# Kernel optimization log

Measured on AMD Instinct MI355X. Metric: run time of the kernel, lower is better.

Reference implementation:

```python
import jax, jax.numpy as jnp
import numpy as np

TWO_PI = 2.0 * np.pi


def setup_inputs() -> dict:
    key = jax.random.key(0)
    ks = jax.random.split(key, 6)
    n1 = n2 = n3 = 20
    nk, ni, nspin = 4, 16, 2
    # Invertible, physically plausible lattice (~8 Bohr cubic cell + jitter)
    A = jnp.eye(3, dtype=jnp.float32) * 8.0 + 0.05 * jax.random.normal(ks[0], (3, 3), jnp.float32)
    k_grid = 0.1 * jax.random.normal(ks[1], (nk, 3), jnp.float32)
    cg_real = jax.random.normal(ks[2], (nspin, nk, ni, n1, n2, n3), jnp.float32)
    cg_imag = jax.random.normal(ks[3], (nspin, nk, ni, n1, n2, n3), jnp.float32)
    # Real-space evaluation grid: fractional coords in [0,1)^3 mapped through A
    frac = jax.random.uniform(ks[4], (n1, n2, n3, 3), jnp.float32)
    r = frac @ A
    return {"A": A, "k_grid": k_grid, "cg_real": cg_real, "cg_imag": cg_imag, "r": r}


def reference(A, k_grid, cg_real, cg_imag, r):
    # cg: [spin, nk, ni, n1, n2, n3] complex plane-wave coefficients
    cg = cg_real + 1j * cg_imag
    n1, n2, n3 = cg.shape[-3:]
    # Integer FFT frequency mesh m -> reciprocal-lattice vectors G = m @ B,
    # B rows are reciprocal basis: B = 2*pi * inv(A)^T  (A rows = lattice vecs)
    f1 = jnp.fft.fftfreq(n1) * n1
    f2 = jnp.fft.fftfreq(n2) * n2
    f3 = jnp.fft.fftfreq(n3) * n3
    m = jnp.stack(jnp.meshgrid(f1, f2, f3, indexing="ij"), axis=-1).astype(A.dtype)  # [n1,n2,n3,3]
    B = TWO_PI * jnp.linalg.inv(A).T
    G = (m @ B).reshape(-1, 3)                      # [nG, 3]
    vol = jnp.abs(jnp.linalg.det(A))
    Rf = r.reshape(-1, 3)                           # [nR, 3]
    # Plane-wave synthesis: psi_{s,k,i}(r) = exp(i k.r)/sqrt(vol) * sum_G c_G exp(i G.r)
    # (equivalent to the triple-nested vmap over the grid dims, fully vectorized)
    phase_g = jnp.exp(1j * (Rf @ G.T))              # [nR, nG] complex
    dens = cg.reshape(*cg.shape[:3], -1)            # [spin, nk, ni, nG]
    psi = jnp.einsum("skin,rn->skir", dens, phase_g)  # [spin, nk, ni, nR]
    phase_k = jnp.exp(1j * (Rf @ k_grid.T))         # [nR, nk]
    psi = psi * jnp.moveaxis(phase_k, 0, -1)[None, :, None, :]
    psi = psi / jnp.sqrt(vol).astype(psi.real.dtype)
    # [spin, nk, ni, n1, n2, n3] -- matches moveaxis(range(3), range(-3,0))
    return psi.reshape(*cg.shape[:3], *r.shape[:-1])
```

## Files before the change

kernel.cpp:

```cpp
#include <hip/hip_runtime.h>

typedef __attribute__((ext_vector_type(4))) float f32x4;
typedef __attribute__((ext_vector_type(8))) short s16x8;

#define NG     8000
#define NRPT   8000
#define NSKIN  128
#define NT     64
#define KK     32
#define KCH    800
#define NKC    10
#define NTILES 25
#define NTOT   (NKC*NTILES)
#define TPB    256
#define WS_TILE_B 16384
#define WS_NEED   ((size_t)NTOT*WS_TILE_B)

__device__ __forceinline__ float sin_rev(float u){ float r; asm("v_sin_f32 %0, %1" : "=v"(r) : "v"(u)); return r; }
__device__ __forceinline__ float cos_rev(float u){ float r; asm("v_cos_f32 %0, %1" : "=v"(r) : "v"(u)); return r; }
__device__ __forceinline__ unsigned int cvt_pk(float lo, float hi){
    unsigned int r; asm("v_cvt_pk_bf16_f32 %0, %1, %2" : "=v"(r) : "v"(lo), "v"(hi)); return r;
}
__device__ __forceinline__ s16x8 bneg(s16x8 v){
    int4 u = *(int4*)&v;
    u.x ^= 0x80008000; u.y ^= 0x80008000; u.z ^= 0x80008000; u.w ^= 0x80008000;
    return *(s16x8*)&u;
}
__device__ __forceinline__ s16x8 pack8(float4 v0, float4 v1){
    union { s16x8 v; uint4 u; } r;
    r.u.x = cvt_pk(v0.x,v0.y); r.u.y = cvt_pk(v0.z,v0.w);
    r.u.z = cvt_pk(v1.x,v1.y); r.u.w = cvt_pk(v1.z,v1.w);
    return r.v;
}
__device__ __forceinline__ int swz(int row, int kg){
    return row*64 + ((kg ^ ((row>>1)&3))<<4);
}

__global__ __launch_bounds__(256) void bloch_prepass(
    const float* __restrict__ cgr, const float* __restrict__ cgi,
    char* __restrict__ ws)
{
    int gid = blockIdx.x*256 + threadIdx.x;
    if (gid >= NTOT*2*8*64) return;
    int lane  = gid & 63;
    int rb8   = (gid >> 6) & 7;
    int plane = (gid >> 9) & 1;
    int tile  = gid >> 10;
    int row   = rb8*16 + (lane & 15);
    int k     = tile*KK + (lane >> 4)*8;
    const float* src = plane ? cgi : cgr;
    const float4 v0 = *(const float4*)&src[(size_t)row*NG + k];
    const float4 v1 = *(const float4*)&src[(size_t)row*NG + k + 4];
    uint4 p;
    p.x = cvt_pk(v0.x, v0.y); p.y = cvt_pk(v0.z, v0.w);
    p.z = cvt_pk(v1.x, v1.y); p.w = cvt_pk(v1.z, v1.w);
    *(uint4*)(ws + (size_t)gid*16) = p;
}

template<bool PRE>
__global__ __launch_bounds__(TPB, 3) void bloch10(
    const float* __restrict__ Amat, const float* __restrict__ kgrid,
    const float* __restrict__ cgr,  const float* __restrict__ cgi,
    const float* __restrict__ rpts, const char* __restrict__ ws,
    float* __restrict__ out, int out_size)
{
    __shared__ __align__(16) char smemB[2*8192];
    __shared__ float fracS[NT][4];
    __shared__ float invAS[9];
    __shared__ float scaleS;

    const int tid = threadIdx.x;
    const int bid = blockIdx.x;
    const int kc  = bid >> 7;
    const int rb  = bid & 127;
    if (rb >= 125) return;
    const int r_base  = rb * NT;
    const int k_begin = kc * KCH;

    if (tid == 0) {
        float a00=Amat[0],a01=Amat[1],a02=Amat[2];
        float a10=Amat[3],a11=Amat[4],a12=Amat[5];
        float a20=Amat[6],a21=Amat[7],a22=Amat[8];
        float c00 =  (a11*a22 - a12*a21);
        float c01 = -(a10*a22 - a12*a20);
        float c02 =  (a10*a21 - a11*a20);
        float det = a00*c00 + a01*c01 + a02*c02;
        float id  = 1.0f/det;
        invAS[0] =  c00*id;
        invAS[1] = -(a01*a22 - a02*a21)*id;
        invAS[2] =  (a01*a12 - a02*a11)*id;
        invAS[3] =  c01*id;
        invAS[4] =  (a00*a22 - a02*a20)*id;
        invAS[5] = -(a00*a12 - a02*a10)*id;
        invAS[6] =  c02*id;
        invAS[7] = -(a00*a21 - a01*a20)*id;
        invAS[8] =  (a00*a11 - a01*a10)*id;
        scaleS   = rsqrtf(fabsf(det));
    }
    __syncthreads();

    if (tid < NT) {
        int rg = r_base + tid;
        float r0 = rpts[rg*3+0], r1 = rpts[rg*3+1], r2 = rpts[rg*3+2];
        fracS[tid][0] = r0*invAS[0] + r1*invAS[3] + r2*invAS[6];
        fracS[tid][1] = r0*invAS[1] + r1*invAS[4] + r2*invAS[7];
        fracS[tid][2] = r0*invAS[2] + r1*invAS[5] + r2*invAS[8];
    }
    __syncthreads();

    f32x4 accRe[4][2], accIm[4][2];
    #pragma unroll
    for (int mi = 0; mi < 4; ++mi)
        #pragma unroll
        for (int ni = 0; ni < 2; ++ni) {
            accRe[mi][ni] = (f32x4){0.f,0.f,0.f,0.f};
            accIm[mi][ni] = (f32x4){0.f,0.f,0.f,0.f};
        }

    const int lane = tid & 63;
    const int wid  = tid >> 6;
    const int wm   = wid >> 1;
    const int wn   = wid & 1;
    const int frow = lane & 15;
    const int kq   = lane >> 4;

    const int sB   = tid >> 2;
    const int qtr  = tid & 3;
    const int stOffB = swz(sB, qtr);
    const int bOff   = swz(wn*32 + frow, kq);

    const float f0r = fracS[sB][0], f1r = fracS[sB][1], f2r = fracS[sB][2];

    float u1 = f2r - floorf(f2r);
    const float w1c = cos_rev(u1), w1s = sin_rev(u1);
    float yd = -20.0f * f2r; yd -= floorf(yd);
    const float wdc = cos_rev(yd), wds = sin_rev(yd);
    const float w1wdc = w1c*wdc - w1s*wds;
    const float w1wds = w1c*wds + w1s*wdc;

    auto stageB = [&](int kb, char* wb){
        int g0   = kb + qtr*8;
        int i12  = (g0 * 3277) >> 16;
        int i3_0 = g0 - i12*20;
        int i1a  = (i12 * 3277) >> 16; int i2a = i12 - i1a*20;
        int i12b = i12 + 1;
        int i1b  = (i12b * 3277) >> 16; int i2b = i12b - i1b*20;
        float m1a = (float)(i1a - (i1a >= 10 ? 20 : 0));
        float m2a = (float)(i2a - (i2a >= 10 ? 20 : 0));
        float m1b = (float)(i1b - (i1b >= 10 ? 20 : 0));
        float m2b = (float)(i2b - (i2b >= 10 ? 20 : 0));
        float m30 = (float)(i3_0 - (i3_0 >= 10 ? 20 : 0));
        float y0 = m1a*f0r + m2a*f1r + m30*f2r; y0 -= floorf(y0);
        float cc = cos_rev(y0), cs = sin_rev(y0);
        float rd = (m1b-m1a)*f0r + (m2b-m2a)*f1r; rd -= floorf(rd);
        float rc = cos_rev(rd), rs = sin_rev(rd);
        float wXc = w1c*rc - w1s*rs;
        float wXs = w1c*rs + w1s*rc;
        float bcv[8], bsv[8];
        bcv[0] = cc; bsv[0] = cs;
        #pragma unroll
        for (int j = 1; j < 8; ++j) {
            bool cB = (i3_0 == 20 - j);
            bool cD = (i3_0 == 10 - j);
            float mc = cB ? wXc : (cD ? w1wdc : w1c);
            float ms = cB ? wXs : (cD ? w1wds : w1s);
            float nc = cc*mc - cs*ms;
            float ns = cc*ms + cs*mc;
            cc = nc; cs = ns;
            bcv[j] = cc; bsv[j] = cs;
        }
        uint4 wc, wsn;
        wc.x  = cvt_pk(bcv[0], bcv[1]); wc.y  = cvt_pk(bcv[2], bcv[3]);
        wc.z  = cvt_pk(bcv[4], bcv[5]); wc.w  = cvt_pk(bcv[6], bcv[7]);
        wsn.x = cvt_pk(bsv[0], bsv[1]); wsn.y = cvt_pk(bsv[2], bsv[3]);
        wsn.z = cvt_pk(bsv[4], bsv[5]); wsn.w = cvt_pk(bsv[6], bsv[7]);
        *(uint4*)(wb +        stOffB) = wc;
        *(uint4*)(wb + 4096 + stOffB) = wsn;
    };

    stageB(k_begin, smemB);
    __syncthreads();

    #pragma unroll 1
    for (int t = 0; t < NTILES; ++t) {
        const int kb = k_begin + t*KK;
        const char* bufP = smemB + (t & 1)*8192;
        char*       bufQ = smemB + ((t + 1) & 1)*8192;

        s16x8 arf[4], aif[4];
        if (PRE) {
            const char* tb = ws + (size_t)(kc*NTILES + t)*WS_TILE_B + lane*16;
            #pragma unroll
            for (int mi = 0; mi < 4; ++mi) {
                arf[mi] = *(const s16x8*)(tb +        (wm*4 + mi)*1024);
                aif[mi] = *(const s16x8*)(tb + 8192 + (wm*4 + mi)*1024);
            }
        } else {
            #pragma unroll
            for (int mi = 0; mi < 4; ++mi) {
                int row = wm*64 + mi*16 + frow;
                int k   = kb + kq*8;
                const float* pr_ = &cgr[(size_t)row*NG + k];
                const float* pi_ = &cgi[(size_t)row*NG + k];
                arf[mi] = pack8(*(const float4*)pr_, *(const float4*)(pr_+4));
                aif[mi] = pack8(*(const float4*)pi_, *(const float4*)(pi_+4));
            }
        }

        s16x8 bcf[2], bsf[2], bsnf[2];
        #pragma unroll
        for (int ni = 0; ni < 2; ++ni) {
            bcf[ni]  = *(const s16x8*)(bufP +        bOff + ni*1024);
            bsf[ni]  = *(const s16x8*)(bufP + 4096 + bOff + ni*1024);
            bsnf[ni] = bneg(bsf[ni]);
        }

        if (t + 1 < NTILES) stageB(kb + KK, bufQ);

        __builtin_amdgcn_s_setprio(1);
        #pragma unroll
        for (int mi = 0; mi < 4; ++mi)
            #pragma unroll
            for (int ni = 0; ni < 2; ++ni) {
                accRe[mi][ni] = __builtin_amdgcn_mfma_f32_16x16x32_bf16(arf[mi], bcf[ni],  accRe[mi][ni], 0, 0, 0);
                accRe[mi][ni] = __builtin_amdgcn_mfma_f32_16x16x32_bf16(aif[mi], bsnf[ni], accRe[mi][ni], 0, 0, 0);
                accIm[mi][ni] = __builtin_amdgcn_mfma_f32_16x16x32_bf16(arf[mi], bsf[ni],  accIm[mi][ni], 0, 0, 0);
                accIm[mi][ni] = __builtin_amdgcn_mfma_f32_16x16x32_bf16(aif[mi], bcf[ni],  accIm[mi][ni], 0, 0, 0);
            }
        __builtin_amdgcn_s_setprio(0);

        __syncthreads();
    }

    float2* ekr = (float2*)smemB;
    {
        int col = tid >> 2, kidx = tid & 3;
        int rg = r_base + col;
        float r0 = rpts[rg*3+0], r1 = rpts[rg*3+1], r2 = rpts[rg*3+2];
        float ang = (r0*kgrid[kidx*3+0] + r1*kgrid[kidx*3+1] + r2*kgrid[kidx*3+2])
                    * 0.15915494309189535f;
        float u = ang - floorf(ang);
        ekr[col*4+kidx] = make_float2(cos_rev(u), sin_rev(u));
    }
    __syncthreads();

    const bool write_imag = (out_size >= 2*NSKIN*NRPT);
    const float scale = scaleS;
    #pragma unroll
    for (int mi = 0; mi < 4; ++mi) {
        const int m0 = wm*64 + mi*16;
        const int kidx = (m0 >> 4) & 3;
        #pragma unroll
        for (int ni = 0; ni < 2; ++ni) {
            int col = wn*32 + ni*16 + frow;
            int rg = r_base + col;
            float2 e = ekr[col*4+kidx];
            float ck = e.x, sk = e.y;
            #pragma unroll
            for (int v = 0; v < 4; ++v) {
                int sg = m0 + kq*4 + v;
                float re = accRe[mi][ni][v];
                float im = accIm[mi][ni][v];
                float orr = (re*ck - im*sk) * scale;
                size_t lin = (size_t)sg * NRPT + rg;
                if (write_imag) {
                    float oi = (re*sk + im*ck) * scale;
                    size_t idx = lin * 2;
                    if (idx + 1 < (size_t)out_size) {
                        atomicAdd(&out[idx],   orr);
                        atomicAdd(&out[idx+1], oi);
                    }
                } else {
                    atomicAdd(&out[lin], orr);
                }
            }
        }
    }
}

extern "C" void kernel_launch(void* const* d_in, const int* in_sizes, int n_in,
                              void* d_out, int out_size, void* d_ws, size_t ws_size,
                              hipStream_t stream) {
    const float* Amat  = (const float*)d_in[0];
    const float* kgrid = (const float*)d_in[1];
    const float* cgr   = (const float*)d_in[2];
    const float* cgi   = (const float*)d_in[3];
    const float* rpts  = (const float*)d_in[4];
    float* out = (float*)d_out;

    hipMemsetAsync(d_out, 0, (size_t)out_size * sizeof(float), stream);

    const bool use_pre = (ws_size >= WS_NEED);
    dim3 grid(NKC * 128);
    if (use_pre) {
        bloch_prepass<<<dim3(NTOT*2*8*64/256), 256, 0, stream>>>(cgr, cgi, (char*)d_ws);
        bloch10<true><<<grid, TPB, 0, stream>>>(Amat, kgrid, cgr, cgi, rpts,
                                                (const char*)d_ws, out, out_size);
    } else {
        bloch10<false><<<grid, TPB, 0, stream>>>(Amat, kgrid, cgr, cgi, rpts,
                                                 nullptr, out, out_size);
    }
}
```

Before: 90.62 us.

## Stage phase factors per G-ring into a six-slot shared ring buffer

Each wave now generates whole rings of 20 contiguous i3 values, one (i1,i2) pair per wave per round. The phases come from one sin/cos seed and a rotation recurrence, which replaces the per-8-element seeding with its extra boundary-correction rotations. Results go into a 6-slot LDS ring, so the kernel syncs once per round of 2-3 tiles instead of once per tile, and the A fragments for the next tile are prefetched into registers. Shared memory grows from 16 KB to 48 KB and launch bounds drop from 3 to 2 blocks, which lowers occupancy. The longer recurrence chain may also lose some bf16/fp32 accuracy.

```diff
diff --git a/kernel.cpp b/kernel.cpp
--- a/kernel.cpp
+++ b/kernel.cpp
@@ -7,14 +7,14 @@
 #define NRPT   8000
 #define NSKIN  128
 #define NT     64
-#define KK     32
 #define KCH    800
 #define NKC    10
 #define NTILES 25
-#define NTOT   (NKC*NTILES)
+#define NROUND 10
+#define NSLOT  6
 #define TPB    256
 #define WS_TILE_B 16384
-#define WS_NEED   ((size_t)NTOT*WS_TILE_B)
+#define WS_NEED   ((size_t)NKC*NTILES*WS_TILE_B)
 
 __device__ __forceinline__ float sin_rev(float u){ float r; asm("v_sin_f32 %0, %1" : "=v"(r) : "v"(u)); return r; }
 __device__ __forceinline__ float cos_rev(float u){ float r; asm("v_cos_f32 %0, %1" : "=v"(r) : "v"(u)); return r; }
@@ -41,13 +41,13 @@
     char* __restrict__ ws)
 {
     int gid = blockIdx.x*256 + threadIdx.x;
-    if (gid >= NTOT*2*8*64) return;
+    if (gid >= NKC*NTILES*2*8*64) return;
     int lane  = gid & 63;
     int rb8   = (gid >> 6) & 7;
     int plane = (gid >> 9) & 1;
     int tile  = gid >> 10;
     int row   = rb8*16 + (lane & 15);
-    int k     = tile*KK + (lane >> 4)*8;
+    int k     = tile*32 + (lane >> 4)*8;
     const float* src = plane ? cgi : cgr;
     const float4 v0 = *(const float4*)&src[(size_t)row*NG + k];
     const float4 v1 = *(const float4*)&src[(size_t)row*NG + k + 4];
@@ -58,13 +58,13 @@
 }
 
 template<bool PRE>
-__global__ __launch_bounds__(TPB, 3) void bloch10(
+__global__ __launch_bounds__(TPB, 2) void bloch12(
     const float* __restrict__ Amat, const float* __restrict__ kgrid,
     const float* __restrict__ cgr,  const float* __restrict__ cgi,
     const float* __restrict__ rpts, const char* __restrict__ ws,
     float* __restrict__ out, int out_size)
 {
-    __shared__ __align__(16) char smemB[2*8192];
+    __shared__ __align__(16) char smem[NSLOT*8192];
     __shared__ float fracS[NT][4];
     __shared__ float invAS[9];
     __shared__ float scaleS;
@@ -74,8 +74,7 @@
     const int kc  = bid >> 7;
     const int rb  = bid & 127;
     if (rb >= 125) return;
-    const int r_base  = rb * NT;
-    const int k_begin = kc * KCH;
+    const int r_base = rb * NT;
 
     if (tid == 0) {
         float a00=Amat[0],a01=Amat[1],a02=Amat[2];
@@ -123,14 +122,9 @@
     const int wn   = wid & 1;
     const int frow = lane & 15;
     const int kq   = lane >> 4;
-
-    const int sB   = tid >> 2;
-    const int qtr  = tid & 3;
-    const int stOffB = swz(sB, qtr);
-    const int bOff   = swz(wn*32 + frow, kq);
-
-    const float f0r = fracS[sB][0], f1r = fracS[sB][1], f2r = fracS[sB][2];
-
+    const int bOff = swz(wn*32 + frow, kq);
+
+    const float f0r = fracS[lane][0], f1r = fracS[lane][1], f2r = fracS[lane][2];
     float u1 = f2r - floorf(f2r);
     const float w1c = cos_rev(u1), w1s = sin_rev(u1);
     float yd = -20.0f * f2r; yd -= floorf(yd);
@@ -138,101 +132,109 @@
     const float w1wdc = w1c*wdc - w1s*wds;
     const float w1wds = w1c*wds + w1s*wdc;
 
-    auto stageB = [&](int kb, char* wb){
-        int g0   = kb + qtr*8;
-        int i12  = (g0 * 3277) >> 16;
-        int i3_0 = g0 - i12*20;
-        int i1a  = (i12 * 3277) >> 16; int i2a = i12 - i1a*20;
-        int i12b = i12 + 1;
-        int i1b  = (i12b * 3277) >> 16; int i2b = i12b - i1b*20;
-        float m1a = (float)(i1a - (i1a >= 10 ? 20 : 0));
-        float m2a = (float)(i2a - (i2a >= 10 ? 20 : 0));
-        float m1b = (float)(i1b - (i1b >= 10 ? 20 : 0));
-        float m2b = (float)(i2b - (i2b >= 10 ? 20 : 0));
-        float m30 = (float)(i3_0 - (i3_0 >= 10 ? 20 : 0));
-        float y0 = m1a*f0r + m2a*f1r + m30*f2r; y0 -= floorf(y0);
+    auto stageRing = [&](int R){
+        int i12 = kc*40 + 4*R + wid;
+        int i1  = (i12 * 3277) >> 16;
+        int i2  = i12 - i1*20;
+        float m1 = (float)(i1 - (i1 >= 10 ? 20 : 0));
+        float m2 = (float)(i2 - (i2 >= 10 ? 20 : 0));
+        float y0 = m1*f0r + m2*f1r; y0 -= floorf(y0);
         float cc = cos_rev(y0), cs = sin_rev(y0);
-        float rd = (m1b-m1a)*f0r + (m2b-m2a)*f1r; rd -= floorf(rd);
-        float rc = cos_rev(rd), rs = sin_rev(rd);
-        float wXc = w1c*rc - w1s*rs;
-        float wXs = w1c*rs + w1s*rc;
-        float bcv[8], bsv[8];
-        bcv[0] = cc; bsv[0] = cs;
+        unsigned int pkc[10], pks[10];
         #pragma unroll
-        for (int j = 1; j < 8; ++j) {
-            bool cB = (i3_0 == 20 - j);
-            bool cD = (i3_0 == 10 - j);
-            float mc = cB ? wXc : (cD ? w1wdc : w1c);
-            float ms = cB ? wXs : (cD ? w1wds : w1s);
-            float nc = cc*mc - cs*ms;
-            float ns = cc*ms + cs*mc;
-            cc = nc; cs = ns;
-            bcv[j] = cc; bsv[j] = cs;
-        }
-        uint4 wc, wsn;
-        wc.x  = cvt_pk(bcv[0], bcv[1]); wc.y  = cvt_pk(bcv[2], bcv[3]);
-        wc.z  = cvt_pk(bcv[4], bcv[5]); wc.w  = cvt_pk(bcv[6], bcv[7]);
-        wsn.x = cvt_pk(bsv[0], bsv[1]); wsn.y = cvt_pk(bsv[2], bsv[3]);
-        wsn.z = cvt_pk(bsv[4], bsv[5]); wsn.w = cvt_pk(bsv[6], bsv[7]);
-        *(uint4*)(wb +        stOffB) = wc;
-        *(uint4*)(wb + 4096 + stOffB) = wsn;
+        for (int jj = 0; jj < 10; ++jj) {
+            float ac = cc, as_ = cs;
+            { float nc = cc*w1c - cs*w1s, ns = cc*w1s + cs*w1c; cc=nc; cs=ns; }
+            pkc[jj] = cvt_pk(ac, cc);
+            pks[jj] = cvt_pk(as_, cs);
+            if (jj < 9) {
+                if (jj == 4) { float nc = cc*w1wdc - cs*w1wds, ns = cc*w1wds + cs*w1wdc; cc=nc; cs=ns; }
+                else         { float nc = cc*w1c  - cs*w1s,  ns = cc*w1s  + cs*w1c;  cc=nc; cs=ns; }
+            }
+        }
+        int gg = (80*R + wid*20) % 192;
+        int gA = gg >> 3;
+        auto adr = [&](int g, int p)->char* {
+            if (g >= 24) g -= 24;
+            return smem + (g>>2)*8192 + p*4096 + swz(lane, g&3);
+        };
+        if ((gg & 7) == 0) {
+            *(uint4*)adr(gA,0)   = make_uint4(pkc[0],pkc[1],pkc[2],pkc[3]);
+            *(uint4*)adr(gA+1,0) = make_uint4(pkc[4],pkc[5],pkc[6],pkc[7]);
+            *(uint2*)adr(gA+2,0) = make_uint2(pkc[8],pkc[9]);
+            *(uint4*)adr(gA,1)   = make_uint4(pks[0],pks[1],pks[2],pks[3]);
+            *(uint4*)adr(gA+1,1) = make_uint4(pks[4],pks[5],pks[6],pks[7]);
+            *(uint2*)adr(gA+2,1) = make_uint2(pks[8],pks[9]);
+        } else {
+            *(uint2*)(adr(gA,0)+8) = make_uint2(pkc[0],pkc[1]);
+            *(uint4*)adr(gA+1,0)   = make_uint4(pkc[2],pkc[3],pkc[4],pkc[5]);
+            *(uint4*)adr(gA+2,0)   = make_uint4(pkc[6],pkc[7],pkc[8],pkc[9]);
+            *(uint2*)(adr(gA,1)+8) = make_uint2(pks[0],pks[1]);
+            *(uint4*)adr(gA+1,1)   = make_uint4(pks[2],pks[3],pks[4],pks[5]);
+            *(uint4*)adr(gA+2,1)   = make_uint4(pks[6],pks[7],pks[8],pks[9]);
+        }
     };
 
-    stageB(k_begin, smemB);
-    __syncthreads();
-
-    #pragma unroll 1
-    for (int t = 0; t < NTILES; ++t) {
-        const int kb = k_begin + t*KK;
-        const char* bufP = smemB + (t & 1)*8192;
-        char*       bufQ = smemB + ((t + 1) & 1)*8192;
-
-        s16x8 arf[4], aif[4];
+    s16x8 arfP[4], aifP[4];
+    auto loadA = [&](int t){
         if (PRE) {
             const char* tb = ws + (size_t)(kc*NTILES + t)*WS_TILE_B + lane*16;
             #pragma unroll
             for (int mi = 0; mi < 4; ++mi) {
-                arf[mi] = *(const s16x8*)(tb +        (wm*4 + mi)*1024);
-                aif[mi] = *(const s16x8*)(tb + 8192 + (wm*4 + mi)*1024);
+                arfP[mi] = *(const s16x8*)(tb +        (wm*4 + mi)*1024);
+                aifP[mi] = *(const s16x8*)(tb + 8192 + (wm*4 + mi)*1024);
             }
         } else {
             #pragma unroll
             for (int mi = 0; mi < 4; ++mi) {
                 int row = wm*64 + mi*16 + frow;
-                int k   = kb + kq*8;
+                int k   = kc*KCH + t*32 + kq*8;
                 const float* pr_ = &cgr[(size_t)row*NG + k];
                 const float* pi_ = &cgi[(size_t)row*NG + k];
-                arf[mi] = pack8(*(const float4*)pr_, *(const float4*)(pr_+4));
-                aif[mi] = pack8(*(const float4*)pi_, *(const float4*)(pi_+4));
-            }
-        }
-
-        s16x8 bcf[2], bsf[2], bsnf[2];
-        #pragma unroll
-        for (int ni = 0; ni < 2; ++ni) {
-            bcf[ni]  = *(const s16x8*)(bufP +        bOff + ni*1024);
-            bsf[ni]  = *(const s16x8*)(bufP + 4096 + bOff + ni*1024);
-            bsnf[ni] = bneg(bsf[ni]);
-        }
-
-        if (t + 1 < NTILES) stageB(kb + KK, bufQ);
-
-        __builtin_amdgcn_s_setprio(1);
-        #pragma unroll
-        for (int mi = 0; mi < 4; ++mi)
+                arfP[mi] = pack8(*(const float4*)pr_, *(const float4*)(pr_+4));
+                aifP[mi] = pack8(*(const float4*)pi_, *(const float4*)(pi_+4));
+            }
+        }
+    };
+
+    loadA(0);
+    stageRing(0);
+    __syncthreads();
+
+    int tcur = 0, slot = 0;
+    #pragma unroll 1
+    for (int R = 0; R < NROUND; ++R) {
+        if (R + 1 < NROUND) stageRing(R + 1);
+        const int t_hi = (5*R + 5) >> 1;
+        #pragma unroll 1
+        while (tcur < t_hi) {
+            const char* base = smem + slot*8192;
+            s16x8 bcf[2], bsf[2], bsnf[2];
             #pragma unroll
             for (int ni = 0; ni < 2; ++ni) {
-                accRe[mi][ni] = __builtin_amdgcn_mfma_f32_16x16x32_bf16(arf[mi], bcf[ni],  accRe[mi][ni], 0, 0, 0);
-                accRe[mi][ni] = __builtin_amdgcn_mfma_f32_16x16x32_bf16(aif[mi], bsnf[ni], accRe[mi][ni], 0, 0, 0);
-                accIm[mi][ni] = __builtin_amdgcn_mfma_f32_16x16x32_bf16(arf[mi], bsf[ni],  accIm[mi][ni], 0, 0, 0);
-                accIm[mi][ni] = __builtin_amdgcn_mfma_f32_16x16x32_bf16(aif[mi], bcf[ni],  accIm[mi][ni], 0, 0, 0);
-            }
-        __builtin_amdgcn_s_setprio(0);
-
+                bcf[ni]  = *(const s16x8*)(base +        bOff + ni*1024);
+                bsf[ni]  = *(const s16x8*)(base + 4096 + bOff + ni*1024);
+                bsnf[ni] = bneg(bsf[ni]);
+            }
+            __builtin_amdgcn_s_setprio(1);
+            #pragma unroll
+            for (int mi = 0; mi < 4; ++mi)
+                #pragma unroll
+                for (int ni = 0; ni < 2; ++ni) {
+                    accRe[mi][ni] = __builtin_amdgcn_mfma_f32_16x16x32_bf16(arfP[mi], bcf[ni],  accRe[mi][ni], 0, 0, 0);
+                    accRe[mi][ni] = __builtin_amdgcn_mfma_f32_16x16x32_bf16(aifP[mi], bsnf[ni], accRe[mi][ni], 0, 0, 0);
+                    accIm[mi][ni] = __builtin_amdgcn_mfma_f32_16x16x32_bf16(arfP[mi], bsf[ni],  accIm[mi][ni], 0, 0, 0);
+                    accIm[mi][ni] = __builtin_amdgcn_mfma_f32_16x16x32_bf16(aifP[mi], bcf[ni],  accIm[mi][ni], 0, 0, 0);
+                }
+            __builtin_amdgcn_s_setprio(0);
+            ++tcur;
+            if (tcur < NTILES) loadA(tcur);
+            ++slot; if (slot == NSLOT) slot = 0;
+        }
         __syncthreads();
     }
 
-    float2* ekr = (float2*)smemB;
+    float2* ekr = (float2*)smem;
     {
         int col = tid >> 2, kidx = tid & 3;
         int rg = r_base + col;
@@ -293,11 +295,11 @@
     const bool use_pre = (ws_size >= WS_NEED);
     dim3 grid(NKC * 128);
     if (use_pre) {
-        bloch_prepass<<<dim3(NTOT*2*8*64/256), 256, 0, stream>>>(cgr, cgi, (char*)d_ws);
-        bloch10<true><<<grid, TPB, 0, stream>>>(Amat, kgrid, cgr, cgi, rpts,
+        bloch_prepass<<<dim3(NKC*NTILES*2*8*64/256), 256, 0, stream>>>(cgr, cgi, (char*)d_ws);
+        bloch12<true><<<grid, TPB, 0, stream>>>(Amat, kgrid, cgr, cgi, rpts,
                                                 (const char*)d_ws, out, out_size);
     } else {
-        bloch10<false><<<grid, TPB, 0, stream>>>(Amat, kgrid, cgr, cgi, rpts,
+        bloch12<false><<<grid, TPB, 0, stream>>>(Amat, kgrid, cgr, cgi, rpts,
                                                  nullptr, out, out_size);
     }
 }
```

New measurement: 89.97 us. About the same (-0.7%).
